# Optimization experiments

Hardware: AMD Instinct MI355X
Metric: run time of the kernel (lower is better)

## Reference

```python
import jax
import jax.numpy as jnp
from jax import lax
import numpy as np

BLANK = 0  # blank label index (init_kwargs)
B, T, U1, V = 8, 128, 65, 1024  # U1 = max_target_len + 1
U = U1 - 1


def setup_inputs() -> dict:
    key = jax.random.key(0)
    k1, k2, k3, k4 = jax.random.split(key, 4)
    logits = jax.random.normal(k1, (B, T, U1, V), dtype=jnp.float32)
    logit_lens = jax.random.randint(k2, (B,), T // 2, T + 1, dtype=jnp.int32)
    # labels cannot be the blank index -> sample from [1, V)
    y = jax.random.randint(k3, (B, U), 1, V, dtype=jnp.int32)
    y_lens = jax.random.randint(k4, (B,), U // 2, U + 1, dtype=jnp.int32)
    return {"logits": logits, "logit_lens": logit_lens, "y": y, "y_lens": y_lens}


def _rnnt_loss(logits, y, logit_lens, y_lens):
    # logits: [B, T, U+1, V]; y: [B, U] int; lengths: [B] int
    logp = jax.nn.log_softmax(logits.astype(jnp.float32), axis=-1)
    lp_blank = logp[..., BLANK]  # [B, T, U+1]
    # label emission logprob at (t, u): logp[b, t, u, y[b, u]] for u < U
    yb = jnp.broadcast_to(y[:, None, :, None].astype(jnp.int32), (B, T, U, 1))
    lp_label = jnp.take_along_axis(logp[:, :, :U, :], yb, axis=3)[..., 0]  # [B, T, U]

    # alpha trellis: alpha[t, u] = logaddexp(alpha[t-1,u] + blank[t-1,u],
    #                                        alpha[t,u-1] + label[t,u-1])
    # init row t = 0: pure label path
    a0 = jnp.concatenate(
        [jnp.zeros((B, 1), jnp.float32), jnp.cumsum(lp_label[:, 0, :], axis=1)], axis=1
    )  # [B, U+1]

    def t_step(prev, inp):
        blank_prev, label_t = inp  # [B, U+1], [B, U]
        c = prev + blank_prev  # vertical (time) transition contribution
        a_first = c[:, 0]  # u = 0: only blank path

        def u_step(carry, xs):
            c_u, l_prev = xs  # each [B]
            a = jnp.logaddexp(c_u, carry + l_prev)
            return a, a

        _, rest = lax.scan(u_step, a_first, (c[:, 1:].T, label_t.T))  # [U, B]
        a = jnp.concatenate([a_first[:, None], rest.T], axis=1)  # [B, U+1]
        return a, a

    _, alphas_rest = lax.scan(
        t_step, a0,
        (jnp.transpose(lp_blank[:, :-1], (1, 0, 2)), jnp.transpose(lp_label[:, 1:], (1, 0, 2))),
    )  # [T-1, B, U+1]
    alphas = jnp.concatenate([a0[None], alphas_rest], axis=0)  # [T, B, U+1]
    alphas = jnp.transpose(alphas, (1, 0, 2))  # [B, T, U+1]

    b_idx = jnp.arange(B)
    t_end = logit_lens.astype(jnp.int32) - 1
    u_end = y_lens.astype(jnp.int32)
    log_like = alphas[b_idx, t_end, u_end] + lp_blank[b_idx, t_end, u_end]
    losses = -log_like  # [B]
    return jnp.mean(losses)  # reduction='mean' over batch


def reference(logits, logit_lens, y, y_lens):
    return _rnnt_loss(logits, y, logit_lens, y_lens)
```

## Files before the change

kernel.cpp:

```cpp
#include <hip/hip_runtime.h>
#include <math.h>

#define BB 8
#define TT 128
#define U1 65
#define UU 64
#define VV 1024
#define DSTR 66
#define NDIAG 208
#define NEGINF -1e30f
#define LOG2E 1.4426950408889634f
#define LN2   0.6931471805599453f

__device__ __forceinline__ float shfl_up1(float x) {
  return __int_as_float(__builtin_amdgcn_update_dpp(
      0, __float_as_int(x), 0x138, 0xf, 0xf, false));
}

__global__ __launch_bounds__(256) void lse_gather(
    const float* __restrict__ logits, const int* __restrict__ y,
    const int* __restrict__ logit_lens, const int* __restrict__ y_lens,
    float* __restrict__ comb, int* __restrict__ done) {
  if (blockIdx.x == 0 && threadIdx.x == 0) *done = 0;

  const int wave = threadIdx.x >> 6;
  const int lane = threadIdx.x & 63;
  const int row  = blockIdx.x * 4 + wave;
  const int u  = row % U1;
  const int bt = row / U1;
  const int b  = bt / TT;
  const int t  = bt % TT;

  float* cb = comb + (size_t)b * NDIAG * DSTR * 2;

  if (lane == 0) {
    if (t == 0) cb[2 * (u * DSTR + u) + 0]   = NEGINF;
    if (u == 0) cb[2 * ((t + 1) * DSTR) + 1] = NEGINF;
  }
  if (t >= logit_lens[b] || u > y_lens[b]) return;

  const float4* rp = (const float4*)(logits + (size_t)row * VV);
  float4 x0 = rp[lane];
  float4 x1 = rp[lane + 64];
  float4 x2 = rp[lane + 128];
  float4 x3 = rp[lane + 192];

  const bool have_label = (u < UU);
  float lab_logit = 0.f;
  if (have_label && lane == 0)
    lab_logit = logits[(size_t)row * VV + y[b * UU + u]];

  float m = fmaxf(fmaxf(fmaxf(x0.x, x0.y), fmaxf(x0.z, x0.w)),
                  fmaxf(fmaxf(x1.x, x1.y), fmaxf(x1.z, x1.w)));
  m = fmaxf(m, fmaxf(fmaxf(fmaxf(x2.x, x2.y), fmaxf(x2.z, x2.w)),
                     fmaxf(fmaxf(x3.x, x3.y), fmaxf(x3.z, x3.w))));
#pragma unroll
  for (int s = 32; s >= 1; s >>= 1) m = fmaxf(m, __shfl_xor(m, s));

  float ss = __expf(x0.x - m) + __expf(x0.y - m) + __expf(x0.z - m) + __expf(x0.w - m)
           + __expf(x1.x - m) + __expf(x1.y - m) + __expf(x1.z - m) + __expf(x1.w - m)
           + __expf(x2.x - m) + __expf(x2.y - m) + __expf(x2.z - m) + __expf(x2.w - m)
           + __expf(x3.x - m) + __expf(x3.y - m) + __expf(x3.z - m) + __expf(x3.w - m);
#pragma unroll
  for (int s = 32; s >= 1; s >>= 1) ss += __shfl_xor(ss, s);

  if (lane == 0) {
    const float lse = m + __logf(ss);
    const int dd = t + u + 1;
    cb[2 * (dd * DSTR + u) + 0] = (x0.x - lse) * LOG2E;
    if (have_label)
      cb[2 * (dd * DSTR + u + 1) + 1] = (lab_logit - lse) * LOG2E;
  }
}

__global__ __launch_bounds__(256) void alpha_dp(
    const float2* __restrict__ comb, const int* __restrict__ logit_lens,
    const int* __restrict__ y_lens, float* __restrict__ losses,
    int* __restrict__ done, float* __restrict__ out) {
  const int b   = blockIdx.x;
  const int tid = threadIdx.x;

  __shared__ __align__(16) float2 cs[NDIAG * DSTR];
  {
    const float4* g = (const float4*)(comb + (size_t)b * NDIAG * DSTR);
    float4* s4 = (float4*)cs;
    for (int i = tid; i < NDIAG * DSTR / 2; i += 256) s4[i] = g[i];
  }
  __syncthreads();
  if (tid >= 64) return;
  const int lane = tid;

  const int tEnd = logit_lens[b] - 1;
  const int uEnd = y_lens[b];
  const int dT   = tEnd + uEnd;

  const float2* cp = cs + lane;
  const float2* ce = cs + 64;

  float M   = (lane == 0) ? 0.f : NEGINF;
  float S   = 1.f;
  float M64 = NEGINF;
  float S64 = 1.f;

#define STEP(cc, ee)                                              \
  {                                                               \
    const float Ml   = shfl_up1(M);                               \
    const float Sl   = shfl_up1(S);    \
    const float mtop = M + (cc).x;                                \
    const float mlft = Ml + (cc).y;                               \
    const float mn   = fmaxf(mtop, mlft);                         \
    const float e1   = __builtin_amdgcn_exp2f(mtop - mn);         \
    const float e2   = __builtin_amdgcn_exp2f(mlft - mn);         \
    const float Sn   = S * e1 + Sl * e2;                          \
    const float mt64 = M64 + (ee).x;                              \
    const float ml64 = M + (ee).y;              \
    const float mn64 = fmaxf(mt64, ml64);                         \
    const float f1   = __builtin_amdgcn_exp2f(mt64 - mn64);       \
    const float f2   = __builtin_amdgcn_exp2f(ml64 - mn64);       \
    S64 = S64 * f1 + S * f2;                    \
    M64 = mn64;                                                   \
    M = mn; S = Sn;                                               \
  }

  float2 c0 = cp[66 * 1], c1 = cp[66 * 2], c2 = cp[66 * 3], c3 = cp[66 * 4],
         c4 = cp[66 * 5], c5 = cp[66 * 6], c6 = cp[66 * 7], c7 = cp[66 * 8];
  float2 e0 = ce[66 * 1], e1_ = ce[66 * 2], e2_ = ce[66 * 3], e3_ = ce[66 * 4],
         e4_ = ce[66 * 5], e5_ = ce[66 * 6], e6_ = ce[66 * 7], e7_ = ce[66 * 8];

  int d = 1;
  for (; d + 7 <= dT; d += 8) {
    const float2 n0 = cp[66 * (d + 8)],  n1 = cp[66 * (d + 9)];
    const float2 n2 = cp[66 * (d + 10)], n3 = cp[66 * (d + 11)];
    const float2 n4 = cp[66 * (d + 12)], n5 = cp[66 * (d + 13)];
    const float2 n6 = cp[66 * (d + 14)], n7 = cp[66 * (d + 15)];
    const float2 f0 = ce[66 * (d + 8)],  f1 = ce[66 * (d + 9)];
    const float2 f2 = ce[66 * (d + 10)], f3 = ce[66 * (d + 11)];
    const float2 f4 = ce[66 * (d + 12)], f5 = ce[66 * (d + 13)];
    const float2 f6 = ce[66 * (d + 14)], f7 = ce[66 * (d + 15)];
    STEP(c0, e0)  STEP(c1, e1_) STEP(c2, e2_) STEP(c3, e3_)
    STEP(c4, e4_) STEP(c5, e5_) STEP(c6, e6_) STEP(c7, e7_)
    c0 = n0; c1 = n1; c2 = n2; c3 = n3; c4 = n4; c5 = n5; c6 = n6; c7 = n7;
    e0 = f0; e1_ = f1; e2_ = f2; e3_ = f3; e4_ = f4; e5_ = f5; e6_ = f6; e7_ = f7;
  }
  if (d <= dT) { STEP(c0, e0)  ++d; }
  if (d <= dT) { STEP(c1, e1_) ++d; }
  if (d <= dT) { STEP(c2, e2_) ++d; }
  if (d <= dT) { STEP(c3, e3_) ++d; }
  if (d <= dT) { STEP(c4, e4_) ++d; }
  if (d <= dT) { STEP(c5, e5_) ++d; }
  if (d <= dT) { STEP(c6, e6_) ++d; }
#undef STEP

  const float Rm = (uEnd == 64) ? M64 : M;
  const float Rs = (uEnd == 64) ? S64 : S;
  const int  sel = (uEnd == 64) ? 63 : uEnd;
  if (lane == sel) {
    const float A = Rm + __builtin_amdgcn_logf(Rs);
    __hip_atomic_store(&losses[b], -(A + cs[(dT + 1) * DSTR + uEnd].x) * LN2,
                       __ATOMIC_RELEASE, __HIP_MEMORY_SCOPE_AGENT);
    const int tk = __hip_atomic_fetch_add(done, 1, __ATOMIC_ACQ_REL,
                                          __HIP_MEMORY_SCOPE_AGENT);
    if (tk == BB - 1) {
      float s = 0.f;
#pragma unroll
      for (int i = 0; i < BB; ++i)
        s += __hip_atomic_load(&losses[i], __ATOMIC_ACQUIRE,
                               __HIP_MEMORY_SCOPE_AGENT);
      out[0] = s * (1.f / BB);
    }
  }
}

extern "C" void kernel_launch(void* const* d_in, const int* in_sizes, int n_in,
                              void* d_out, int out_size, void* d_ws, size_t ws_size,
                              hipStream_t stream) {
  const float* logits     = (const float*)d_in[0];
  const int*   logit_lens = (const int*)d_in[1];
  const int*   y          = (const int*)d_in[2];
  const int*   y_lens     = (const int*)d_in[3];
  float* out = (float*)d_out;

  float2* comb   = (float2*)d_ws;
  float*  losses = (float*)(comb + (size_t)BB * NDIAG * DSTR);
  int*    done   = (int*)(losses + BB);

  const int rows = BB * TT * U1;
  lse_gather<<<rows / 4, 256, 0, stream>>>(logits, y, logit_lens, y_lens,
                                           (float*)comb, done);
  alpha_dp<<<BB, 256, 0, stream>>>(comb, logit_lens, y_lens, losses, done, out);
}
```

Measured before the change: 48.67 us.

## Run alpha DP in linear probability space with periodic exponent rescaling

The producer kernel now stores emission probabilities (exp(x-m)/sum) instead of log2-probabilities, and the serial anti-diagonal DP multiplies and adds plain values instead of doing max/exp2 log-sum-exp with separate mantissa and scale. Every four diagonals a reference lane's float exponent is read and all values are rescaled by a power of two, with the exponent kept in an integer counter. This removes four exp2 calls and several max/sub operations from each serial DP step. In exchange it adds a readlane and branch per rescale, and it can lose precision or underflow if values along a diagonal span more than the float range relative to the chosen reference lane.

```diff
diff --git a/kernel.cpp b/kernel.cpp
--- a/kernel.cpp
+++ b/kernel.cpp
@@ -9,7 +9,6 @@
 #define DSTR 66
 #define NDIAG 208
 #define NEGINF -1e30f
-#define LOG2E 1.4426950408889634f
 #define LN2   0.6931471805599453f
 
 __device__ __forceinline__ float shfl_up1(float x) {
@@ -34,8 +33,8 @@
   float* cb = comb + (size_t)b * NDIAG * DSTR * 2;
 
   if (lane == 0) {
-    if (t == 0) cb[2 * (u * DSTR + u) + 0]   = NEGINF;
-    if (u == 0) cb[2 * ((t + 1) * DSTR) + 1] = NEGINF;
+    if (t == 0) cb[2 * (u * DSTR + u) + 0]   = 0.f;
+    if (u == 0) cb[2 * ((t + 1) * DSTR) + 1] = 0.f;
   }
   if (t >= logit_lens[b] || u > y_lens[b]) return;
 
@@ -65,11 +64,11 @@
   for (int s = 32; s >= 1; s >>= 1) ss += __shfl_xor(ss, s);
 
   if (lane == 0) {
-    const float lse = m + __logf(ss);
+    const float rss = __builtin_amdgcn_rcpf(ss);
     const int dd = t + u + 1;
-    cb[2 * (dd * DSTR + u) + 0] = (x0.x - lse) * LOG2E;
+    cb[2 * (dd * DSTR + u) + 0] = __expf(x0.x - m) * rss;
     if (have_label)
-      cb[2 * (dd * DSTR + u + 1) + 1] = (lab_logit - lse) * LOG2E;
+      cb[2 * (dd * DSTR + u + 1) + 1] = __expf(lab_logit - m) * rss;
   }
 }
 
@@ -93,33 +92,33 @@
   const int tEnd = logit_lens[b] - 1;
   const int uEnd = y_lens[b];
   const int dT   = tEnd + uEnd;
+  const int uclamp = (uEnd < 63) ? uEnd : 63;
 
   const float2* cp = cs + lane;
   const float2* ce = cs + 64;
 
-  float M   = (lane == 0) ? 0.f : NEGINF;
-  float S   = 1.f;
-  float M64 = NEGINF;
-  float S64 = 1.f;
+  float V    = (lane == 0) ? 1.f : 0.f;
+  float V64  = 0.f;
+  int   Rexp = 0;
 
-#define STEP(cc, ee)                                              \
-  {                                                               \
-    const float Ml   = shfl_up1(M);                               \
-    const float Sl   = shfl_up1(S);    \
-    const float mtop = M + (cc).x;                                \
-    const float mlft = Ml + (cc).y;                               \
-    const float mn   = fmaxf(mtop, mlft);                         \
-    const float e1   = __builtin_amdgcn_exp2f(mtop - mn);         \
-    const float e2   = __builtin_amdgcn_exp2f(mlft - mn);         \
-    const float Sn   = S * e1 + Sl * e2;                          \
-    const float mt64 = M64 + (ee).x;                              \
-    const float ml64 = M + (ee).y;              \
-    const float mn64 = fmaxf(mt64, ml64);                         \
-    const float f1   = __builtin_amdgcn_exp2f(mt64 - mn64);       \
-    const float f2   = __builtin_amdgcn_exp2f(ml64 - mn64);       \
-    S64 = S64 * f1 + S * f2;                    \
-    M64 = mn64;                                                   \
-    M = mn; S = Sn;                                               \
+#define STEP(cc, ee)                                      \
+  {                                                       \
+    const float Vl  = shfl_up1(V);                        \
+    const float t64 = V * (ee).y;       \
+    V   = V * (cc).x + Vl * (cc).y;                       \
+    V64 = V64 * (ee).x + t64;                             \
+  }
+
+#define RESCALE(dd)                                                     \
+  {                                                                     \
+    const int ref = min(max((dd) - (tEnd >> 1), 0), uclamp);            \
+    const float vr = __int_as_float(                                    \
+        __builtin_amdgcn_readlane(__float_as_int(V), ref));             \
+    const int eb = (__float_as_int(vr) >> 23) & 0xff;                   \
+    if (eb > 0 && eb < 255) {                                           \
+      const float sc = __int_as_float((254 - eb) << 23);   \
+      V *= sc; V64 *= sc; Rexp += eb - 127;                             \
+    }                                                                   \
   }
 
   float2 c0 = cp[66 * 1], c1 = cp[66 * 2], c2 = cp[66 * 3], c3 = cp[66 * 4],
@@ -138,26 +137,29 @@
     const float2 f4 = ce[66 * (d + 12)], f5 = ce[66 * (d + 13)];
     const float2 f6 = ce[66 * (d + 14)], f7 = ce[66 * (d + 15)];
     STEP(c0, e0)  STEP(c1, e1_) STEP(c2, e2_) STEP(c3, e3_)
+    RESCALE(d + 3)
     STEP(c4, e4_) STEP(c5, e5_) STEP(c6, e6_) STEP(c7, e7_)
+    RESCALE(d + 7)
     c0 = n0; c1 = n1; c2 = n2; c3 = n3; c4 = n4; c5 = n5; c6 = n6; c7 = n7;
     e0 = f0; e1_ = f1; e2_ = f2; e3_ = f3; e4_ = f4; e5_ = f5; e6_ = f6; e7_ = f7;
   }
-  if (d <= dT) { STEP(c0, e0)  ++d; }
-  if (d <= dT) { STEP(c1, e1_) ++d; }
-  if (d <= dT) { STEP(c2, e2_) ++d; }
-  if (d <= dT) { STEP(c3, e3_) ++d; }
-  if (d <= dT) { STEP(c4, e4_) ++d; }
-  if (d <= dT) { STEP(c5, e5_) ++d; }
-  if (d <= dT) { STEP(c6, e6_) ++d; }
+  if (d <= dT) { STEP(c0, e0)  RESCALE(d) ++d; }
+  if (d <= dT) { STEP(c1, e1_) RESCALE(d) ++d; }
+  if (d <= dT) { STEP(c2, e2_) RESCALE(d) ++d; }
+  if (d <= dT) { STEP(c3, e3_) RESCALE(d) ++d; }
+  if (d <= dT) { STEP(c4, e4_) RESCALE(d) ++d; }
+  if (d <= dT) { STEP(c5, e5_) RESCALE(d) ++d; }
+  if (d <= dT) { STEP(c6, e6_) RESCALE(d) ++d; }
 #undef STEP
+#undef RESCALE
 
-  const float Rm = (uEnd == 64) ? M64 : M;
-  const float Rs = (uEnd == 64) ? S64 : S;
-  const int  sel = (uEnd == 64) ? 63 : uEnd;
+  const float Vres = (uEnd == 64) ? V64 : V;
+  const int  sel   = (uEnd == 64) ? 63 : uEnd;
   if (lane == sel) {
-    const float A = Rm + __builtin_amdgcn_logf(Rs);
-    __hip_atomic_store(&losses[b], -(A + cs[(dT + 1) * DSTR + uEnd].x) * LN2,
-                       __ATOMIC_RELEASE, __HIP_MEMORY_SCOPE_AGENT);
+    const float a = (float)Rexp + __builtin_amdgcn_logf(Vres)
+                  + __builtin_amdgcn_logf(cs[(dT + 1) * DSTR + uEnd].x);
+    __hip_atomic_store(&losses[b], -a * LN2, __ATOMIC_RELEASE,
+                       __HIP_MEMORY_SCOPE_AGENT);
     const int tk = __hip_atomic_fetch_add(done, 1, __ATOMIC_ACQ_REL,
                                           __HIP_MEMORY_SCOPE_AGENT);
     if (tk == BB - 1) {
```

Result: faster. 45.60 us (-6.3%).
